# Optimization experiments

Hardware: AMD Instinct MI355X
Metric: run time of the kernel (lower is better)

## Reference

```python
import jax, jax.numpy as jnp
import numpy as np

DIM = 256      # channel dim
NW = 7         # n_win per side
HEADS = 8
TOPK = 4
KVW = 4        # kv_per_win (ada_avgpool output side)
EPS = 1e-6


def _dwconv(x, w, b):
    # depthwise conv, NHWC, 'SAME' == padding k//2 for odd kernels
    y = jax.lax.conv_general_dilated(
        x, w, (1, 1), 'SAME',
        dimension_numbers=('NHWC', 'HWIO', 'NHWC'),
        feature_group_count=x.shape[-1])
    return y + b


def _ln(x, g, b):
    mu = x.mean(-1, keepdims=True)
    var = ((x - mu) ** 2).mean(-1, keepdims=True)
    return (x - mu) * jax.lax.rsqrt(var + EPS) * g + b


def _bra(x, qkv_w, qkv_b, wo_w, wo_b, lepe_w, lepe_b):
    # BiLevelRoutingAttention, x: (n, H, W, C)
    n, H, W, C = x.shape
    hw, ww = H // NW, W // NW          # window size (8, 8)
    scale = C ** -0.5                   # qk_dim ** -0.5 (BiFormer uses full qk_dim)
    qkv = x @ qkv_w.T + qkv_b           # (n, H, W, 3C)
    # window partition: n (j hw) (i ww) c -> n (j i) hw ww c
    qkv_win = qkv.reshape(n, NW, hw, NW, ww, 3 * C)
    qkv_win = qkv_win.transpose(0, 1, 3, 2, 4, 5).reshape(n, NW * NW, hw, ww, 3 * C)
    q = qkv_win[..., :C]                # (n, p2, hw, ww, C)
    kv = qkv_win[..., C:]               # (n, p2, hw, ww, 2C)
    # --- window-level routing (q/k detached in torch; no fwd effect) ---
    q_win = q.mean((2, 3))              # (n, p2, C)
    k_win = kv[..., :C].mean((2, 3))    # (n, p2, C)
    logits = jnp.einsum('npc,nqc->npq', q_win * scale, k_win)
    _, idx = jax.lax.top_k(logits, TOPK)            # (n, p2, k)
    # --- kv downsample: adaptive avg pool (hw,ww)->(KVW,KVW), exact 2x2 mean here ---
    fh, fw = hw // KVW, ww // KVW
    kv_pix = kv.reshape(n, NW * NW, KVW, fh, KVW, fw, 2 * C).mean((3, 5))
    kv_pix = kv_pix.reshape(n, NW * NW, KVW * KVW, 2 * C)   # (n, p2, w2, 2C)
    # --- gather top-k windows' kv ---
    kv_sel = jax.vmap(lambda t, ix: t[ix])(kv_pix, idx)     # (n, p2, k, w2, 2C)
    cph = C // HEADS
    k_sel = kv_sel[..., :C].reshape(n, NW * NW, TOPK * KVW * KVW, HEADS, cph)
    v_sel = kv_sel[..., C:].reshape(n, NW * NW, TOPK * KVW * KVW, HEADS, cph)
    q_pix = q.reshape(n, NW * NW, hw * ww, HEADS, cph)
    # --- windowed attention over gathered tokens ---
    att = jnp.einsum('npqmc,npsmc->npmqs', q_pix * scale, k_sel)
    att = jax.nn.softmax(att, axis=-1)
    out = jnp.einsum('npmqs,npsmc->npqmc', att, v_sel)
    out = out.reshape(n, NW, NW, hw, ww, C).transpose(0, 1, 3, 2, 4, 5).reshape(n, H, W, C)
    # --- lepe: depthwise 5x5 on v over the full image ---
    v_img = qkv[..., 2 * C:]
    out = out + _dwconv(v_img, lepe_w, lepe_b)
    return out @ wo_w.T + wo_b


def setup_inputs() -> dict:
    key = jax.random.key(0)
    ks = jax.random.split(key, 8)
    C, s = DIM, 0.02
    p = {}
    p['x'] = jax.random.normal(ks[0], (16, C, 56, 56), jnp.float32)
    p['pos_w'] = jax.random.normal(ks[1], (3, 3, 1, C), jnp.float32) * s
    p['pos_b'] = jnp.zeros((C,), jnp.float32)
    p['ln1_g'] = jnp.ones((C,), jnp.float32)
    p['ln1_b'] = jnp.zeros((C,), jnp.float32)
    p['ln2_g'] = jnp.ones((C,), jnp.float32)
    p['ln2_b'] = jnp.zeros((C,), jnp.float32)
    p['qkv_w'] = jax.random.normal(ks[2], (3 * C, C), jnp.float32) * s
    p['qkv_b'] = jnp.zeros((3 * C,), jnp.float32)
    p['wo_w'] = jax.random.normal(ks[3], (C, C), jnp.float32) * s
    p['wo_b'] = jnp.zeros((C,), jnp.float32)
    p['lepe_w'] = jax.random.normal(ks[4], (5, 5, 1, C), jnp.float32) * s
    p['lepe_b'] = jnp.zeros((C,), jnp.float32)
    p['fc1_w'] = jax.random.normal(ks[5], (4 * C, C), jnp.float32) * s
    p['fc1_b'] = jnp.zeros((4 * C,), jnp.float32)
    p['fc2_w'] = jax.random.normal(ks[6], (C, 4 * C), jnp.float32) * s
    p['fc2_b'] = jnp.zeros((C,), jnp.float32)
    return p


def reference(x, pos_w, pos_b, ln1_g, ln1_b, ln2_g, ln2_b, qkv_w, qkv_b,
              wo_w, wo_b, lepe_w, lepe_b, fc1_w, fc1_b, fc2_w, fc2_b):
    xh = x.transpose(0, 2, 3, 1)                       # NCHW -> NHWC
    xh = xh + _dwconv(xh, pos_w, pos_b)                # pos embed (dw 3x3)
    xh = xh + _bra(_ln(xh, ln1_g, ln1_b), qkv_w, qkv_b, wo_w, wo_b, lepe_w, lepe_b)
    h = _ln(xh, ln2_g, ln2_b)
    h = jax.nn.gelu(h @ fc1_w.T + fc1_b, approximate=False)
    xh = xh + (h @ fc2_w.T + fc2_b)
    return xh.transpose(0, 3, 1, 2)                    # NHWC -> NCHW
```

## Files before the change

### kernel.cpp

```cpp
#include <hip/hip_runtime.h>
#include <math.h>

static constexpr int NIMG = 16;
static constexpr int TOK  = NIMG * 56 * 56;
static constexpr size_t TC = (size_t)TOK * 256;
static constexpr int PTOK = 784 * 16;

typedef __bf16 bf16x8 __attribute__((ext_vector_type(8)));
typedef float  f32x4  __attribute__((ext_vector_type(4)));

__device__ inline float bf2f(unsigned short u) {
  unsigned int i = ((unsigned int)u) << 16; float f; __builtin_memcpy(&f, &i, 4); return f;
}
__device__ inline unsigned short f2bf(float f) {
  unsigned int i; __builtin_memcpy(&i, &f, 4);
  unsigned int r = i + 0x7fffu + ((i >> 16) & 1u);
  return (unsigned short)(r >> 16);
}

__global__ __launch_bounds__(256) void nchw2nhwc(const float* __restrict__ x,
                                                 float* __restrict__ y) {
  __shared__ float T[32][37];
  int nh = blockIdx.z;
  int n = nh / 56, h = nh % 56;
  int c0 = blockIdx.y * 32, w0 = blockIdx.x * 32;
  int tid = threadIdx.x;
  int wlim = 56 - w0; if (wlim > 32) wlim = 32;
  {
    int ci = tid >> 3, w = (tid & 7) * 4;
    if (w < wlim) {
      f32x4 v = *(const f32x4*)&x[(((size_t)n * 256 + c0 + ci) * 56 + h) * 56 + w0 + w];
#pragma unroll
      for (int j = 0; j < 4; j++) T[ci][w + j] = v[j];
    }
  }
  __syncthreads();
  {
    int wi = tid >> 3, cq = tid & 7;
    if (wi < wlim) {
      f32x4 o;
#pragma unroll
      for (int k = 0; k < 4; k++) o[k] = T[cq * 4 + k][wi];
      *(f32x4*)&y[(((size_t)n * 56 + h) * 56 + w0 + wi) * 256 + c0 + cq * 4] = o;
    }
  }
}

__global__ __launch_bounds__(256) void nhwc2nchw(const float* __restrict__ y,
                                                 float* __restrict__ o) {
  __shared__ float T[32][37];
  int nh = blockIdx.z;
  int n = nh / 56, h = nh % 56;
  int w0 = blockIdx.x * 32, c0 = blockIdx.y * 32;
  int tid = threadIdx.x;
  int wlim = 56 - w0; if (wlim > 32) wlim = 32;
  {
    int wi = tid >> 3, cq = tid & 7;
    if (wi < wlim) {
      f32x4 v = *(const f32x4*)&y[(((size_t)n * 56 + h) * 56 + w0 + wi) * 256 + c0 + cq * 4];
#pragma unroll
      for (int k = 0; k < 4; k++) T[wi][cq * 4 + k] = v[k];
    }
  }
  __syncthreads();
  {
    int ci = tid >> 3, w = (tid & 7) * 4;
    if (w < wlim) {
      f32x4 ov;
#pragma unroll
      for (int j = 0; j < 4; j++) ov[j] = T[w + j][ci];
      *(f32x4*)&o[(((size_t)n * 256 + c0 + ci) * 56 + h) * 56 + w0 + w] = ov;
    }
  }
}

__global__ __launch_bounds__(256) void posln_kernel(const float* __restrict__ xt,
                                                    const float* __restrict__ w,
                                                    const float* __restrict__ bb,
                                                    const float* __restrict__ g1,
                                                    const float* __restrict__ b1,
                                                    float* __restrict__ xh,
                                                    unsigned short* __restrict__ lnb,
                                                    float* __restrict__ murs) {
  int bid = blockIdx.x;
  int wgid = (bid & 7) * 1568 + (bid >> 3);
  int t = wgid * 4 + (threadIdx.x >> 6);
  int lane = threadIdx.x & 63;
  int c = lane * 4;
  int n = t / 3136, rem = t % 3136, h = rem / 56, ww = rem % 56;
  const float* base = xt + (size_t)n * 3136 * 256 + c;

  f32x4 xx[9]; float msk[9];
#pragma unroll
  for (int k = 0; k < 9; k++) {
    int dh = k / 3 - 1, dw = k % 3 - 1;
    int hh = h + dh, wc = ww + dw;
    msk[k] = ((unsigned)hh < 56u && (unsigned)wc < 56u) ? 1.f : 0.f;
    int hcl = hh < 0 ? 0 : (hh > 55 ? 55 : hh);
    int wcl = wc < 0 ? 0 : (wc > 55 ? 55 : wc);
    xx[k] = *(const f32x4*)&base[(size_t)(hcl * 56 + wcl) * 256];
  }
  f32x4 acc = *(const f32x4*)&bb[c];
#pragma unroll
  for (int k = 0; k < 9; k++) {
    f32x4 wv = *(const f32x4*)&w[k * 256 + c];
    acc += xx[k] * (wv * msk[k]);
  }
  f32x4 v = xx[4] + acc;
  *(f32x4*)&xh[(size_t)t * 256 + c] = v;

  float s = v[0] + v[1] + v[2] + v[3];
#pragma unroll
  for (int m = 1; m < 64; m <<= 1) s += __shfl_xor(s, m);
  float mu = s * (1.f / 256.f);
  f32x4 d = v - mu;
  float ss = d[0] * d[0] + d[1] * d[1] + d[2] * d[2] + d[3] * d[3];
#pragma unroll
  for (int m = 1; m < 64; m <<= 1) ss += __shfl_xor(ss, m);
  float rs = rsqrtf(ss * (1.f / 256.f) + 1e-6f);
  f32x4 gg = *(const f32x4*)&g1[c];
  f32x4 b4 = *(const f32x4*)&b1[c];
  f32x4 y = d * rs * gg + b4;
  unsigned short yb[4];
#pragma unroll
  for (int j = 0; j < 4; j++) yb[j] = f2bf(y[j]);
  __builtin_memcpy(lnb + (size_t)t * 256 + c, yb, 8);
  if (lane == 0) {
    murs[2 * (size_t)t] = mu;
    murs[2 * (size_t)t + 1] = rs;
  }
}

template <bool OUTBF, bool LN2F>
__global__ __launch_bounds__(512, 4) void mgemm2(const unsigned short* __restrict__ A, int lda,
                                                 const unsigned short* __restrict__ B, int ldb,
                                                 const float* __restrict__ bias,
                                                 const float* __restrict__ R,
                                                 void* __restrict__ C_,
                                                 int N, int K, int flags, int gx,
                                                 const float* __restrict__ g2,
                                                 const float* __restrict__ b2,
                                                 unsigned short* __restrict__ ob2) {
  __shared__ unsigned short As[128 * 64];
  __shared__ unsigned short Bs[256 * 64];
  __shared__ float redS[4][128];
  __shared__ float redQ[4][128];
  int tid = threadIdx.x;
  int nwg = gridDim.x, bid = blockIdx.x;
  int q8 = nwg >> 3, r8 = nwg & 7;
  int xcd = bid & 7, pos = bid >> 3;
  int wgid = (xcd < r8 ? xcd * (q8 + 1) : r8 * (q8 + 1) + (xcd - r8) * q8) + pos;
  int m0 = (wgid / gx) * 128;
  int n0 = (wgid % gx) * 256;

  int lane = tid & 63, wid = tid >> 6;
  int wr = (wid >> 2) * 64, wc = (wid & 3) * 64;
  int llo = lane & 15, lhi = lane >> 4;

  f32x4 acc[4][4];
#pragma unroll
  for (int i = 0; i < 4; i++)
#pragma unroll
    for (int j = 0; j < 4; j++) acc[i][j] = (f32x4){0.f, 0.f, 0.f, 0.f};

  for (int k0 = 0; k0 < K; k0 += 64) {
#pragma unroll
    for (int i = 0; i < 2; i++) {
      int qa = tid + 512 * i;
      int row = qa >> 3, col = (qa & 7) ^ (row & 7);
      __builtin_amdgcn_global_load_lds(
          (const __attribute__((address_space(1))) unsigned int*)
              (A + (size_t)(m0 + row) * lda + k0 + col * 8),
          (__attribute__((address_space(3))) unsigned int*)(As + qa * 8), 16, 0, 0);
    }
#pragma unroll
    for (int i = 0; i < 4; i++) {
      int qb = tid + 512 * i;
      int row = qb >> 3, col = (qb & 7) ^ (row & 7);
      __builtin_amdgcn_global_load_lds(
          (const __attribute__((address_space(1))) unsigned int*)
              (B + (size_t)(n0 + row) * ldb + k0 + col * 8),
          (__attribute__((address_space(3))) unsigned int*)(Bs + qb * 8), 16, 0, 0);
    }
    __syncthreads();
#pragma unroll
    for (int ks = 0; ks < 2; ks++) {
      int cchunk = ks * 4 + lhi;
      bf16x8 af[4], bfr[4];
#pragma unroll
      for (int mi = 0; mi < 4; mi++) {
        int r = wr + mi * 16 + llo;
        __builtin_memcpy(&af[mi], As + (size_t)r * 64 + (cchunk ^ (r & 7)) * 8, 16);
      }
#pragma unroll
      for (int nj = 0; nj < 4; nj++) {
        int r = wc + nj * 16 + llo;
        __builtin_memcpy(&bfr[nj], Bs + (size_t)r * 64 + (cchunk ^ (r & 7)) * 8, 16);
      }
#pragma unroll
      for (int mi = 0; mi < 4; mi++)
#pragma unroll
        for (int nj = 0; nj < 4; nj++)
          acc[mi][nj] = __builtin_amdgcn_mfma_f32_16x16x32_bf16(af[mi], bfr[nj],
                                                                acc[mi][nj], 0, 0, 0);
    }
    __syncthreads();
  }

  if constexpr (LN2F) {
    float sr[4][4], qr[4][4];
#pragma unroll
    for (int mi = 0; mi < 4; mi++)
#pragma unroll
      for (int j = 0; j < 4; j++) { sr[mi][j] = 0.f; qr[mi][j] = 0.f; }
#pragma unroll
    for (int mi = 0; mi < 4; mi++)
#pragma unroll
      for (int nj = 0; nj < 4; nj++) {
        int n = wc + nj * 16 + llo;
        float bv = bias[n];
#pragma unroll
        for (int j = 0; j < 4; j++) {
          int m = m0 + wr + mi * 16 + lhi * 4 + j;
          float v = acc[mi][nj][j] + bv + R[(size_t)m * 256 + n];
          acc[mi][nj][j] = v;
          sr[mi][j] += v;
          qr[mi][j] += v * v;
        }
      }
#pragma unroll
    for (int mi = 0; mi < 4; mi++)
#pragma unroll
      for (int j = 0; j < 4; j++)
#pragma unroll
        for (int d = 1; d < 16; d <<= 1) {
          sr[mi][j] += __shfl_xor(sr[mi][j], d);
          qr[mi][j] += __shfl_xor(qr[mi][j], d);
        }
    if (llo == 0) {
#pragma unroll
      for (int mi = 0; mi < 4; mi++)
#pragma unroll
        for (int j = 0; j < 4; j++) {
          int lr = wr + mi * 16 + lhi * 4 + j;
          redS[wid & 3][lr] = sr[mi][j];
          redQ[wid & 3][lr] = qr[mi][j];
        }
    }
    __syncthreads();
#pragma unroll
    for (int mi = 0; mi < 4; mi++)
#pragma unroll
      for (int j = 0; j < 4; j++) {
        int lr = wr + mi * 16 + lhi * 4 + j;
        float S = redS[0][lr] + redS[1][lr] + redS[2][lr] + redS[3][lr];
        float Q = redQ[0][lr] + redQ[1][lr] + redQ[2][lr] + redQ[3][lr];
        float mu = S * (1.f / 256.f);
        float var = Q * (1.f / 256.f) - mu * mu;
        float rs = rsqrtf(var + 1e-6f);
        size_t mrow = (size_t)(m0 + lr) * 256;
#pragma unroll
        for (int nj = 0; nj < 4; nj++) {
          int n = wc + nj * 16 + llo;
          float v = acc[mi][nj][j];
          ((float*)C_)[mrow + n] = v;
          ob2[mrow + n] = f2bf((v - mu) * rs * g2[n] + b2[n]);
        }
      }
  } else {
    int coln = llo, rowg = lhi * 4;
#pragma unroll
    for (int mi = 0; mi < 4; mi++) {
#pragma unroll
      for (int nj = 0; nj < 4; nj++) {
        int n = n0 + wc + nj * 16 + coln;
        float bv = (flags & 8) ? 0.f : bias[n];
#pragma unroll
        for (int j = 0; j < 4; j++) {
          int m = m0 + wr + mi * 16 + rowg + j;
          float v = acc[mi][nj][j] + bv;
          if (flags & 1) v = 0.5f * v * (1.0f + erff(v * 0.70710678118654752f));
          if (flags & 2) v += R[(size_t)m * N + n];
          if (OUTBF) ((unsigned short*)C_)[(size_t)m * N + n] = f2bf(v);
          else       ((float*)C_)[(size_t)m * N + n] = v;
        }
      }
    }
  }
}

__global__ __launch_bounds__(256) void prep_kernel(const float* __restrict__ qkv_w,
                                                   const float* __restrict__ qkv_b,
                                                   const float* __restrict__ wo_w,
                                                   const float* __restrict__ fc1_w,
                                                   const float* __restrict__ fc2_w,
                                                   unsigned short* __restrict__ wqv,
                                                   unsigned short* __restrict__ wkv,
                                                   unsigned short* __restrict__ wwo,
                                                   unsigned short* __restrict__ wfc1,
                                                   unsigned short* __restrict__ wfc2,
                                                   float* __restrict__ bqv) {
  int i = blockIdx.x * 256 + threadIdx.x;
  if (i < 65536) { wqv[i] = f2bf(qkv_w[i]); }
  else if (i < 131072) { int j = i - 65536; wqv[65536 + j] = f2bf(qkv_w[512 * 256 + j]); }
  else if (i < 262144) { int j = i - 131072; wkv[j] = f2bf(qkv_w[256 * 256 + j]); }
  else if (i < 327680) { int j = i - 262144; wwo[j] = f2bf(wo_w[j]); }
  else if (i < 589824) { int j = i - 327680; wfc1[j] = f2bf(fc1_w[j]); }
  else if (i < 851968) { int j = i - 589824; wfc2[j] = f2bf(fc2_w[j]); }
  else if (i < 852480) { int j = i - 851968; bqv[j] = qkv_b[j < 256 ? j : j + 256]; }
}

__global__ __launch_bounds__(256) void pool_kernel(const float* __restrict__ xh,
                                                   const float* __restrict__ murs,
                                                   const float* __restrict__ g1,
                                                   const float* __restrict__ b1,
                                                   unsigned short* __restrict__ plx,
                                                   float* __restrict__ wmx) {
  int np = blockIdx.x * 4 + (threadIdx.x >> 6);
  int lane = threadIdx.x & 63;
  int c = lane * 4;
  int n = np / 49, p = np % 49, wr = p / 7, wcq = p % 7;
  f32x4 g4 = *(const f32x4*)&g1[c];
  f32x4 b4 = *(const f32x4*)&b1[c];
  f32x4 tot = (f32x4){0.f, 0.f, 0.f, 0.f};
  for (int s = 0; s < 16; s++) {
    int i = s >> 2, j = s & 3;
    f32x4 z = (f32x4){0.f, 0.f, 0.f, 0.f};
    for (int di = 0; di < 2; di++)
      for (int dj = 0; dj < 2; dj++) {
        size_t t = ((size_t)n * 56 + wr * 8 + i * 2 + di) * 56 + wcq * 8 + j * 2 + dj;
        float mu = murs[2 * t], rs = murs[2 * t + 1];
        f32x4 v = *(const f32x4*)&xh[t * 256 + c];
        z += (v - mu) * rs;
      }
    z *= 0.25f;
    f32x4 cell = z * g4 + b4;
    unsigned short ab[4];
#pragma unroll
    for (int k = 0; k < 4; k++) ab[k] = f2bf(cell[k]);
    __builtin_memcpy(plx + ((size_t)np * 16 + s) * 256 + c, ab, 8);
    tot += z;
  }
  f32x4 wm = tot * (1.f / 16.f) * g4 + b4;
  *(f32x4*)&wmx[(size_t)np * 256 + c] = wm;
}

__global__ __launch_bounds__(256) void winproj_kernel(const float* __restrict__ wmx,
                                                      const float* __restrict__ qkv_w,
                                                      const float* __restrict__ qkv_b,
                                                      float* __restrict__ qkwin) {
  int np = blockIdx.x, t = threadIdx.x;
  __shared__ float xs[256];
  xs[t] = wmx[(size_t)np * 256 + t];
  __syncthreads();
  for (int rep = 0; rep < 2; rep++) {
    int n = t + rep * 256;
    const float* wrow = qkv_w + (size_t)n * 256;
    float s = qkv_b[n];
    for (int c = 0; c < 256; c++) s += xs[c] * wrow[c];
    qkwin[(size_t)np * 512 + n] = s;
  }
}

__global__ __launch_bounds__(64) void topk_kernel(const float* __restrict__ qkwin,
                                                  int* __restrict__ idx) {
  int np = blockIdx.x;
  int n = np / 49;
  int j = threadIdx.x;
  __shared__ float lg[49];
  if (j < 49) {
    const float* qp = qkwin + (size_t)np * 512;
    const float* kp = qkwin + ((size_t)n * 49 + j) * 512 + 256;
    float s = 0.f;
    for (int c = 0; c < 256; c++) s += qp[c] * kp[c];
    lg[j] = s;
  }
  __syncthreads();
  if (j == 0) {
    unsigned long long used = 0ull;
    for (int t = 0; t < 4; t++) {
      float best = -INFINITY;
      int bi = 0;
      for (int q = 0; q < 49; q++)
        if (!((used >> q) & 1ull) && lg[q] > best) { best = lg[q]; bi = q; }
      idx[np * 4 + t] = bi;
      used |= (1ull << bi);
    }
  }
}

__global__ __launch_bounds__(64) void attn_mfma(const unsigned short* __restrict__ qvb,
                                                const unsigned short* __restrict__ kvp,
                                                const int* __restrict__ idx,
                                                unsigned short* __restrict__ out) {
  __shared__ unsigned short Vt[32 * 72];
  __shared__ unsigned short Pl[64 * 72];
  int bid = blockIdx.x;
  int head = bid & 7, np = bid >> 3;
  int n = np / 49, p = np % 49;
  int h0 = (p / 7) * 8, w0 = (p % 7) * 8;
  int lane = threadIdx.x;
  int lhi = lane >> 4, llo = lane & 15;

  int wi4[4];
#pragma unroll
  for (int t = 0; t < 4; t++) wi4[t] = idx[np * 4 + t];

#pragma unroll
  for (int it = 0; it < 4; it++) {
    int cell = lane >> 2;
    int chunk = lane & 3;
    int s = it * 16 + cell;
    const unsigned short* g = kvp + ((size_t)(n * 49 + wi4[it]) * 16 + cell) * 512
                              + 256 + head * 32 + chunk * 8;
    unsigned short vv[8];
    __builtin_memcpy(vv, g, 16);
#pragma unroll
    for (int j = 0; j < 8; j++) Vt[(chunk * 8 + j) * 72 + s] = vv[j];
  }

  bf16x8 qf[4], kf[4];
#pragma unroll
  for (int mi = 0; mi < 4; mi++) {
    int row = mi * 16 + llo;
    int h = h0 + (row >> 3), w = w0 + (row & 7);
    __builtin_memcpy(&qf[mi],
                     qvb + (((size_t)n * 56 + h) * 56 + w) * 512 + head * 32 + lhi * 8, 16);
  }
#pragma unroll
  for (int nj = 0; nj < 4; nj++) {
    __builtin_memcpy(&kf[nj],
                     kvp + ((size_t)(n * 49 + wi4[nj]) * 16 + llo) * 512 + head * 32 + lhi * 8,
                     16);
  }

  f32x4 acc[4][4];
#pragma unroll
  for (int mi = 0; mi < 4; mi++)
#pragma unroll
    for (int nj = 0; nj < 4; nj++) acc[mi][nj] = (f32x4){0.f, 0.f, 0.f, 0.f};
#pragma unroll
  for (int mi = 0; mi < 4; mi++)
#pragma unroll
    for (int nj = 0; nj < 4; nj++)
      acc[mi][nj] = __builtin_amdgcn_mfma_f32_16x16x32_bf16(qf[mi], kf[nj], acc[mi][nj], 0, 0, 0);

#pragma unroll
  for (int mi = 0; mi < 4; mi++)
#pragma unroll
    for (int nj = 0; nj < 4; nj++) acc[mi][nj] *= 0.0625f;
#pragma unroll
  for (int mi = 0; mi < 4; mi++) {
#pragma unroll
    for (int reg = 0; reg < 4; reg++) {
      float m = fmaxf(fmaxf(acc[mi][0][reg], acc[mi][1][reg]),
                      fmaxf(acc[mi][2][reg], acc[mi][3][reg]));
      m = fmaxf(m, __shfl_xor(m, 1));
      m = fmaxf(m, __shfl_xor(m, 2));
      m = fmaxf(m, __shfl_xor(m, 4));
      m = fmaxf(m, __shfl_xor(m, 8));
      float sum = 0.f;
#pragma unroll
      for (int nj = 0; nj < 4; nj++) {
        float e = __expf(acc[mi][nj][reg] - m);
        acc[mi][nj][reg] = e;
        sum += e;
      }
      sum += __shfl_xor(sum, 1);
      sum += __shfl_xor(sum, 2);
      sum += __shfl_xor(sum, 4);
      sum += __shfl_xor(sum, 8);
      float inv = 1.0f / sum;
#pragma unroll
      for (int nj = 0; nj < 4; nj++) acc[mi][nj][reg] *= inv;
    }
  }

#pragma unroll
  for (int mi = 0; mi < 4; mi++)
#pragma unroll
    for (int nj = 0; nj < 4; nj++)
#pragma unroll
      for (int reg = 0; reg < 4; reg++) {
        int row = mi * 16 + lhi * 4 + reg;
        Pl[row * 72 + nj * 16 + llo] = f2bf(acc[mi][nj][reg]);
      }

  f32x4 o[4][2];
#pragma unroll
  for (int mi = 0; mi < 4; mi++)
#pragma unroll
    for (int nc = 0; nc < 2; nc++) o[mi][nc] = (f32x4){0.f, 0.f, 0.f, 0.f};
#pragma unroll
  for (int ks = 0; ks < 2; ks++) {
    bf16x8 pa[4], vb[2];
#pragma unroll
    for (int mi = 0; mi < 4; mi++)
      __builtin_memcpy(&pa[mi], Pl + (mi * 16 + llo) * 72 + ks * 32 + lhi * 8, 16);
#pragma unroll
    for (int nc = 0; nc < 2; nc++)
      __builtin_memcpy(&vb[nc], Vt + (nc * 16 + llo) * 72 + ks * 32 + lhi * 8, 16);
#pragma unroll
    for (int mi = 0; mi < 4; mi++)
#pragma unroll
      for (int nc = 0; nc < 2; nc++)
        o[mi][nc] = __builtin_amdgcn_mfma_f32_16x16x32_bf16(pa[mi], vb[nc], o[mi][nc], 0, 0, 0);
  }

#pragma unroll
  for (int mi = 0; mi < 4; mi++)
#pragma unroll
    for (int nc = 0; nc < 2; nc++)
#pragma unroll
      for (int reg = 0; reg < 4; reg++) {
        int row = mi * 16 + lhi * 4 + reg;
        int h = h0 + (row >> 3), w = w0 + (row & 7);
        out[(((size_t)n * 56 + h) * 56 + w) * 256 + head * 32 + nc * 16 + llo] =
            f2bf(o[mi][nc][reg]);
      }
}

__global__ __launch_bounds__(256) void lepe_kernel(const unsigned short* __restrict__ qvb,
                                                   const float* __restrict__ w,
                                                   const float* __restrict__ b,
                                                   unsigned short* __restrict__ out) {
  int bid = blockIdx.x;
  int wgid = (bid & 7) * 784 + (bid >> 3);
  int t = wgid * 8 + (threadIdx.x >> 5);
  int cg = threadIdx.x & 31;
  int c = cg * 8;
  int n = t / 3136, rem = t % 3136, h = rem / 56, ww = rem % 56;
  const unsigned short* vbase = qvb + (size_t)n * 3136 * 512 + 256 + c;

  unsigned short vv[25][8];
  float msk[25];
#pragma unroll
  for (int k = 0; k < 25; k++) {
    int dh = k / 5 - 2, dw = k % 5 - 2;
    int hh = h + dh, wc = ww + dw;
    msk[k] = ((unsigned)hh < 56u && (unsigned)wc < 56u) ? 1.f : 0.f;
    int hcl = hh < 0 ? 0 : (hh > 55 ? 55 : hh);
    int wcl = wc < 0 ? 0 : (wc > 55 ? 55 : wc);
    __builtin_memcpy(&vv[k][0], vbase + (size_t)(hcl * 56 + wcl) * 512, 16);
  }

  float acc[8];
#pragma unroll
  for (int j = 0; j < 8; j++) acc[j] = b[c + j];
#pragma unroll
  for (int k = 0; k < 25; k++) {
    const float* wp = w + k * 256 + c;
#pragma unroll
    for (int j = 0; j < 8; j++) acc[j] += bf2f(vv[k][j]) * (wp[j] * msk[k]);
  }

  size_t o = (size_t)t * 256 + c;
  unsigned short ov[8];
  __builtin_memcpy(ov, out + o, 16);
#pragma unroll
  for (int j = 0; j < 8; j++) ov[j] = f2bf(bf2f(ov[j]) + acc[j]);
  __builtin_memcpy(out + o, ov, 16);
}

extern "C" void kernel_launch(void* const* d_in, const int* in_sizes, int n_in,
                              void* d_out, int out_size, void* d_ws, size_t ws_size,
                              hipStream_t stream) {
  const float* x      = (const float*)d_in[0];
  const float* pos_w  = (const float*)d_in[1];
  const float* pos_b  = (const float*)d_in[2];
  const float* ln1_g  = (const float*)d_in[3];
  const float* ln1_b  = (const float*)d_in[4];
  const float* ln2_g  = (const float*)d_in[5];
  const float* ln2_b  = (const float*)d_in[6];
  const float* qkv_w  = (const float*)d_in[7];
  const float* qkv_b  = (const float*)d_in[8];
  const float* wo_w   = (const float*)d_in[9];
  const float* wo_b   = (const float*)d_in[10];
  const float* lepe_w = (const float*)d_in[11];
  const float* lepe_b = (const float*)d_in[12];
  const float* fc1_w  = (const float*)d_in[13];
  const float* fc1_b  = (const float*)d_in[14];
  const float* fc2_w  = (const float*)d_in[15];
  const float* fc2_b  = (const float*)d_in[16];

  float*          xt   = (float*)d_out;
  unsigned short* qvb  = (unsigned short*)d_out;
  unsigned short* hbuf = (unsigned short*)d_out;

  float*          r2   = (float*)d_ws;
  float*          wmx  = r2 + TC;
  float*          qkw  = wmx + (size_t)784 * 256;
  float*          bqv  = qkw + (size_t)784 * 512;
  unsigned short* lnb  = (unsigned short*)(bqv + 512);
  unsigned short* aob  = lnb;
  unsigned short* ln2b = lnb;
  unsigned short* plx  = lnb + TC;
  unsigned short* kvp  = plx + (size_t)PTOK * 256;
  unsigned short* wqv  = kvp + (size_t)PTOK * 512;
  unsigned short* wkv  = wqv + (size_t)512 * 256;
  unsigned short* wwo  = wkv + (size_t)512 * 256;
  unsigned short* wfc1 = wwo + (size_t)256 * 256;
  unsigned short* wfc2 = wfc1 + (size_t)1024 * 256;
  int*            idx  = (int*)(wfc2 + (size_t)256 * 1024);
  float*          murs = (float*)(idx + 784 * 4);

  prep_kernel<<<3330, 256, 0, stream>>>(qkv_w, qkv_b, wo_w, fc1_w, fc2_w,
                                        wqv, wkv, wwo, wfc1, wfc2, bqv);
  nchw2nhwc<<<dim3(2, 8, NIMG * 56), 256, 0, stream>>>(x, xt);
  posln_kernel<<<TOK / 4, 256, 0, stream>>>(xt, pos_w, pos_b, ln1_g, ln1_b,
                                            r2, lnb, murs);
  pool_kernel<<<196, 256, 0, stream>>>(r2, murs, ln1_g, ln1_b, plx, wmx);
  mgemm2<true, false><<<784, 512, 0, stream>>>(lnb, 256, wqv, 256, bqv, nullptr,
                                               qvb, 512, 256, 0, 2,
                                               nullptr, nullptr, nullptr);
  mgemm2<true, false><<<196, 512, 0, stream>>>(plx, 256, wkv, 256, qkv_b + 256, nullptr,
                                               kvp, 512, 256, 0, 2,
                                               nullptr, nullptr, nullptr);
  winproj_kernel<<<784, 256, 0, stream>>>(wmx, qkv_w, qkv_b, qkw);
  topk_kernel<<<784, 64, 0, stream>>>(qkw, idx);
  attn_mfma<<<6272, 64, 0, stream>>>(qvb, kvp, idx, aob);
  lepe_kernel<<<TOK / 8, 256, 0, stream>>>(qvb, lepe_w, lepe_b, aob);
  mgemm2<false, true><<<392, 512, 0, stream>>>(aob, 256, wwo, 256, wo_b, r2,
                                               r2, 256, 256, 2, 1,
                                               ln2_g, ln2_b, ln2b);
  mgemm2<true, false><<<784, 512, 0, stream>>>(ln2b, 256, wfc1, 256, fc1_b, nullptr,
                                               hbuf, 512, 256, 1, 2,
                                               nullptr, nullptr, nullptr);
  mgemm2<false, false><<<392, 512, 0, stream>>>(hbuf, 512, wfc2, 1024, fc2_b, r2,
                                                r2, 256, 512, 2, 1,
                                                nullptr, nullptr, nullptr);
  mgemm2<true, false><<<784, 512, 0, stream>>>(ln2b, 256, wfc1 + (size_t)512 * 256, 256,
                                               fc1_b + 512, nullptr,
                                               hbuf, 512, 256, 1, 2,
                                               nullptr, nullptr, nullptr);
  mgemm2<false, false><<<392, 512, 0, stream>>>(hbuf, 512, wfc2 + 512, 1024, fc2_b, r2,
                                                r2, 256, 512, 2 | 8, 1,
                                                nullptr, nullptr, nullptr);
  nhwc2nchw<<<dim3(2, 8, NIMG * 56), 256, 0, stream>>>(r2, (float*)d_out);
}
```

Measured before the change: 479.5 us.

## Stage GEMM and attention epilogues through LDS for coalesced vector stores

```diff
diff --git a/kernel.cpp b/kernel.cpp
--- a/kernel.cpp
+++ b/kernel.cpp
@@ -141,10 +141,12 @@
                                                  const float* __restrict__ g2,
                                                  const float* __restrict__ b2,
                                                  unsigned short* __restrict__ ob2) {
-  __shared__ unsigned short As[128 * 64];
-  __shared__ unsigned short Bs[256 * 64];
-  __shared__ float redS[4][128];
-  __shared__ float redQ[4][128];
+  __shared__ __attribute__((aligned(16))) char smraw[49152];
+  unsigned short* As = (unsigned short*)smraw;
+  unsigned short* Bs = (unsigned short*)(smraw + 16384);
+  float* slab = (float*)smraw;
+  constexpr int SSTR = 260;
+
   int tid = threadIdx.x;
   int nwg = gridDim.x, bid = blockIdx.x;
   int q8 = nwg >> 3, r8 = nwg & 7;
@@ -207,85 +209,83 @@
     __syncthreads();
   }
 
-  if constexpr (LN2F) {
-    float sr[4][4], qr[4][4];
-#pragma unroll
-    for (int mi = 0; mi < 4; mi++)
-#pragma unroll
-      for (int j = 0; j < 4; j++) { sr[mi][j] = 0.f; qr[mi][j] = 0.f; }
-#pragma unroll
-    for (int mi = 0; mi < 4; mi++)
-#pragma unroll
-      for (int nj = 0; nj < 4; nj++) {
-        int n = wc + nj * 16 + llo;
-        float bv = bias[n];
-#pragma unroll
-        for (int j = 0; j < 4; j++) {
-          int m = m0 + wr + mi * 16 + lhi * 4 + j;
-          float v = acc[mi][nj][j] + bv + R[(size_t)m * 256 + n];
-          acc[mi][nj][j] = v;
-          sr[mi][j] += v;
-          qr[mi][j] += v * v;
+#pragma unroll
+  for (int s = 0; s < 4; s++) {
+    if (wr == (s >> 1) * 64) {
+#pragma unroll
+      for (int mi2 = 0; mi2 < 2; mi2++) {
+        int mi = (s & 1) * 2 + mi2;
+#pragma unroll
+        for (int nj = 0; nj < 4; nj++) {
+          int col = wc + nj * 16 + llo;
+#pragma unroll
+          for (int j = 0; j < 4; j++)
+            slab[(mi2 * 16 + lhi * 4 + j) * SSTR + col] = acc[mi][nj][j];
         }
       }
-#pragma unroll
-    for (int mi = 0; mi < 4; mi++)
-#pragma unroll
-      for (int j = 0; j < 4; j++)
-#pragma unroll
-        for (int d = 1; d < 16; d <<= 1) {
-          sr[mi][j] += __shfl_xor(sr[mi][j], d);
-          qr[mi][j] += __shfl_xor(qr[mi][j], d);
+    }
+    __syncthreads();
+    int gmBase = m0 + s * 32;
+    if (OUTBF) {
+#pragma unroll
+      for (int i2 = 0; i2 < 2; i2++) {
+        int rr = wid * 4 + i2 * 2 + (lane >> 5);
+        int col = (lane & 31) * 8;
+        f32x4 v0 = *(f32x4*)&slab[rr * SSTR + col];
+        f32x4 v1 = *(f32x4*)&slab[rr * SSTR + col + 4];
+        if (!(flags & 8)) {
+          v0 += *(const f32x4*)&bias[n0 + col];
+          v1 += *(const f32x4*)&bias[n0 + col + 4];
         }
-    if (llo == 0) {
-#pragma unroll
-      for (int mi = 0; mi < 4; mi++)
-#pragma unroll
-        for (int j = 0; j < 4; j++) {
-          int lr = wr + mi * 16 + lhi * 4 + j;
-          redS[wid & 3][lr] = sr[mi][j];
-          redQ[wid & 3][lr] = qr[mi][j];
+        if (flags & 1) {
+#pragma unroll
+          for (int j = 0; j < 4; j++) {
+            v0[j] = 0.5f * v0[j] * (1.0f + erff(v0[j] * 0.70710678118654752f));
+            v1[j] = 0.5f * v1[j] * (1.0f + erff(v1[j] * 0.70710678118654752f));
+          }
         }
+        unsigned short ob[8];
+#pragma unroll
+        for (int j = 0; j < 4; j++) { ob[j] = f2bf(v0[j]); ob[4 + j] = f2bf(v1[j]); }
+        __builtin_memcpy((unsigned short*)C_ + (size_t)(gmBase + rr) * N + n0 + col, ob, 16);
+      }
+    } else {
+#pragma unroll
+      for (int i = 0; i < 4; i++) {
+        int rr = wid * 4 + i;
+        int gm = gmBase + rr;
+        int col = lane * 4;
+        f32x4 v = *(f32x4*)&slab[rr * SSTR + col];
+        if (!(flags & 8)) v += *(const f32x4*)&bias[n0 + col];
+        if (flags & 1) {
+#pragma unroll
+          for (int j = 0; j < 4; j++)
+            v[j] = 0.5f * v[j] * (1.0f + erff(v[j] * 0.70710678118654752f));
+        }
+        if (flags & 2) v += *(const f32x4*)&R[(size_t)gm * N + n0 + col];
+        if (LN2F) {
+          float sv = v[0] + v[1] + v[2] + v[3];
+          float qv = v[0] * v[0] + v[1] * v[1] + v[2] * v[2] + v[3] * v[3];
+#pragma unroll
+          for (int d = 1; d < 64; d <<= 1) {
+            sv += __shfl_xor(sv, d);
+            qv += __shfl_xor(qv, d);
+          }
+          float mu = sv * (1.f / 256.f);
+          float var = qv * (1.f / 256.f) - mu * mu;
+          float rs = rsqrtf(var + 1e-6f);
+          f32x4 g4 = *(const f32x4*)&g2[col];
+          f32x4 b4 = *(const f32x4*)&b2[col];
+          f32x4 y = (v - mu) * rs * g4 + b4;
+          unsigned short yb[4];
+#pragma unroll
+          for (int j = 0; j < 4; j++) yb[j] = f2bf(y[j]);
+          __builtin_memcpy(ob2 + (size_t)gm * 256 + col, yb, 8);
+        }
+        *(f32x4*)&((float*)C_)[(size_t)gm * N + n0 + col] = v;
+      }
     }
     __syncthreads();
-#pragma unroll
-    for (int mi = 0; mi < 4; mi++)
-#pragma unroll
-      for (int j = 0; j < 4; j++) {
-        int lr = wr + mi * 16 + lhi * 4 + j;
-        float S = redS[0][lr] + redS[1][lr] + redS[2][lr] + redS[3][lr];
-        float Q = redQ[0][lr] + redQ[1][lr] + redQ[2][lr] + redQ[3][lr];
-        float mu = S * (1.f / 256.f);
-        float var = Q * (1.f / 256.f) - mu * mu;
-        float rs = rsqrtf(var + 1e-6f);
-        size_t mrow = (size_t)(m0 + lr) * 256;
-#pragma unroll
-        for (int nj = 0; nj < 4; nj++) {
-          int n = wc + nj * 16 + llo;
-          float v = acc[mi][nj][j];
-          ((float*)C_)[mrow + n] = v;
-          ob2[mrow + n] = f2bf((v - mu) * rs * g2[n] + b2[n]);
-        }
-      }
-  } else {
-    int coln = llo, rowg = lhi * 4;
-#pragma unroll
-    for (int mi = 0; mi < 4; mi++) {
-#pragma unroll
-      for (int nj = 0; nj < 4; nj++) {
-        int n = n0 + wc + nj * 16 + coln;
-        float bv = (flags & 8) ? 0.f : bias[n];
-#pragma unroll
-        for (int j = 0; j < 4; j++) {
-          int m = m0 + wr + mi * 16 + rowg + j;
-          float v = acc[mi][nj][j] + bv;
-          if (flags & 1) v = 0.5f * v * (1.0f + erff(v * 0.70710678118654752f));
-          if (flags & 2) v += R[(size_t)m * N + n];
-          if (OUTBF) ((unsigned short*)C_)[(size_t)m * N + n] = f2bf(v);
-          else       ((float*)C_)[(size_t)m * N + n] = v;
-        }
-      }
-    }
   }
 }
 
@@ -507,6 +507,7 @@
         o[mi][nc] = __builtin_amdgcn_mfma_f32_16x16x32_bf16(pa[mi], vb[nc], o[mi][nc], 0, 0, 0);
   }
 
+  __syncthreads();
 #pragma unroll
   for (int mi = 0; mi < 4; mi++)
 #pragma unroll
@@ -514,10 +515,18 @@
 #pragma unroll
       for (int reg = 0; reg < 4; reg++) {
         int row = mi * 16 + lhi * 4 + reg;
-        int h = h0 + (row >> 3), w = w0 + (row & 7);
-        out[(((size_t)n * 56 + h) * 56 + w) * 256 + head * 32 + nc * 16 + llo] =
-            f2bf(o[mi][nc][reg]);
-      }
+        Pl[row * 40 + nc * 16 + llo] = f2bf(o[mi][nc][reg]);
+      }
+  __syncthreads();
+#pragma unroll
+  for (int it = 0; it < 4; it++) {
+    int slot = it * 64 + lane;
+    int row = slot >> 2, cp = slot & 3;
+    unsigned short ov[8];
+    __builtin_memcpy(ov, Pl + row * 40 + cp * 8, 16);
+    int h = h0 + (row >> 3), w = w0 + (row & 7);
+    __builtin_memcpy(out + (((size_t)n * 56 + h) * 56 + w) * 256 + head * 32 + cp * 8, ov, 16);
+  }
 }
 
 __global__ __launch_bounds__(256) void lepe_kernel(const unsigned short* __restrict__ qvb,
@@ -532,26 +541,21 @@
   int n = t / 3136, rem = t % 3136, h = rem / 56, ww = rem % 56;
   const unsigned short* vbase = qvb + (size_t)n * 3136 * 512 + 256 + c;
 
-  unsigned short vv[25][8];
-  float msk[25];
+  float acc[8];
+#pragma unroll
+  for (int j = 0; j < 8; j++) acc[j] = b[c + j];
 #pragma unroll
   for (int k = 0; k < 25; k++) {
     int dh = k / 5 - 2, dw = k % 5 - 2;
     int hh = h + dh, wc = ww + dw;
-    msk[k] = ((unsigned)hh < 56u && (unsigned)wc < 56u) ? 1.f : 0.f;
+    float msk = ((unsigned)hh < 56u && (unsigned)wc < 56u) ? 1.f : 0.f;
     int hcl = hh < 0 ? 0 : (hh > 55 ? 55 : hh);
     int wcl = wc < 0 ? 0 : (wc > 55 ? 55 : wc);
-    __builtin_memcpy(&vv[k][0], vbase + (size_t)(hcl * 56 + wcl) * 512, 16);
-  }
-
-  float acc[8];
-#pragma unroll
-  for (int j = 0; j < 8; j++) acc[j] = b[c + j];
-#pragma unroll
-  for (int k = 0; k < 25; k++) {
+    unsigned short vv[8];
+    __builtin_memcpy(vv, vbase + (size_t)(hcl * 56 + wcl) * 512, 16);
     const float* wp = w + k * 256 + c;
 #pragma unroll
-    for (int j = 0; j < 8; j++) acc[j] += bf2f(vv[k][j]) * (wp[j] * msk[k]);
+    for (int j = 0; j < 8; j++) acc[j] += bf2f(vv[j]) * (wp[j] * msk);
   }
 
   size_t o = (size_t)t * 256 + c;
```

Result: faster. 447.3 us (-6.7%).
